# Performance work log

Measured on AMD Instinct MI355X. Metric: run time of the kernel, lower is better.

Reference implementation:

```python
import jax, jax.numpy as jnp
import numpy as np

D, H, NL, P, HP = 768, 12, 12, 16, 14          # hidden, heads, layers, patch, patches-per-side
NPATCH = HP * HP                                # 196
DH = D // H
EPS = 1e-6                                      # torchvision ViT LayerNorm eps


def _ln(x, s, b):
    m = jnp.mean(x, -1, keepdims=True)
    v = jnp.mean((x - m) ** 2, -1, keepdims=True)
    return (x - m) * jax.lax.rsqrt(v + EPS) * s + b


def _attn(x, wqkv, bqkv, wo, bo):
    B, L, _ = x.shape
    qkv = x @ wqkv + bqkv
    q, k, v = [t.reshape(B, L, H, DH) for t in jnp.split(qkv, 3, axis=-1)]
    s = jnp.einsum('bqhd,bkhd->bhqk', q, k) / np.float32(np.sqrt(DH))
    w = jax.nn.softmax(s, axis=-1)              # [B,H,L,L] per-head attn weights
    o = jnp.einsum('bhqk,bkhd->bqhd', w, v).reshape(B, L, D)
    return o @ wo + bo, w


def _block(x, i, ln1_s, ln1_b, qkv_w, qkv_b, proj_w, proj_b, ln2_s, ln2_b, mlp_w1, mlp_b1, mlp_w2, mlp_b2):
    a, _ = _attn(_ln(x, ln1_s[i], ln1_b[i]), qkv_w[i], qkv_b[i], proj_w[i], proj_b[i])
    x = x + a
    h = _ln(x, ln2_s[i], ln2_b[i])
    h = jax.nn.gelu(h @ mlp_w1[i] + mlp_b1[i], approximate=False) @ mlp_w2[i] + mlp_b2[i]
    return x + h


def setup_inputs():
    key = jax.random.key(0)
    ks = jax.random.split(key, 10)
    B, sd = 32, 0.02
    f = lambda kk, sh: jax.random.normal(kk, sh, jnp.float32) * sd
    return dict(
        x=jax.random.normal(ks[0], (B, 3, 224, 224), jnp.float32),
        conv_w=f(ks[1], (D, 3, P, P)),
        conv_b=jnp.zeros((D,), jnp.float32),
        cls_tok=f(ks[2], (1, 1, D)),
        pos_emb=f(ks[3], (1, NPATCH + 1, D)),
        ln1_s=jnp.ones((NL, D), jnp.float32), ln1_b=jnp.zeros((NL, D), jnp.float32),
        qkv_w=f(ks[4], (NL, D, 3 * D)), qkv_b=jnp.zeros((NL, 3 * D), jnp.float32),
        proj_w=f(ks[5], (NL, D, D)), proj_b=jnp.zeros((NL, D), jnp.float32),
        ln2_s=jnp.ones((NL, D), jnp.float32), ln2_b=jnp.zeros((NL, D), jnp.float32),
        mlp_w1=f(ks[6], (NL, D, 4 * D)), mlp_b1=jnp.zeros((NL, 4 * D), jnp.float32),
        mlp_w2=f(ks[7], (NL, 4 * D, D)), mlp_b2=jnp.zeros((NL, D), jnp.float32),
        fln_s=jnp.ones((D,), jnp.float32), fln_b=jnp.zeros((D,), jnp.float32),
        imp_w=f(ks[8], (D, 1)), imp_b=jnp.zeros((1,), jnp.float32),
        k=100,
    )


def reference(x, conv_w, conv_b, cls_tok, pos_emb, ln1_s, ln1_b, qkv_w, qkv_b,
              proj_w, proj_b, ln2_s, ln2_b, mlp_w1, mlp_b1, mlp_w2, mlp_b2,
              fln_s, fln_b, imp_w, imp_b, k):
    B = x.shape[0]
    # conv_proj (stride==kernel==16) as patchify + GEMM
    p = x.reshape(B, 3, HP, P, HP, P).transpose(0, 2, 4, 1, 3, 5).reshape(B, NPATCH, 3 * P * P)
    t = p @ conv_w.reshape(D, -1).T + conv_b
    t = jnp.concatenate([jnp.broadcast_to(cls_tok, (B, 1, D)), t], axis=1) + pos_emb
    blk = lambda xx, i: _block(xx, i, ln1_s, ln1_b, qkv_w, qkv_b, proj_w, proj_b,
                               ln2_s, ln2_b, mlp_w1, mlp_b1, mlp_w2, mlp_b2)
    for i in range(NL - 1):
        t = blk(t, i)
    # eager re-run of penultimate layer's self-attention on x (no pre-LN, per source)
    _, w = _attn(t, qkv_w[NL - 2], qkv_b[NL - 2], proj_w[NL - 2], proj_b[NL - 2])
    A_hat = w[:, :, 0, 1:].sum(axis=1)                       # [B, NPATCH] cls-row attn summed over heads
    patches = t[:, 1:, :]
    Z = jax.nn.sigmoid(patches @ imp_w + imp_b)[..., 0]
    O = A_hat + A_hat * Z
    _, idx = jax.lax.top_k(O, k)                             # indices (sorted desc; source uses sorted=False)
    gidx = jnp.broadcast_to(idx[:, :, None], (B, k, D))
    top_patches = jnp.take_along_axis(patches, gidx, axis=1)
    pos_full = jnp.broadcast_to(pos_emb, (B, NPATCH + 1, D))
    top_pos = jnp.take_along_axis(pos_full[:, 1:, :], gidx, axis=1)
    inp = jnp.concatenate([t[:, :1, :], top_patches], axis=1) + \
          jnp.concatenate([pos_full[:, :1, :], top_pos], axis=1)
    out = blk(inp, NL - 1)
    out = _ln(out, fln_s, fln_b)
    return out, top_patches
```

## Files before the change

### kernel.cpp

```cpp
#include <hip/hip_runtime.h>
#include <hip/hip_fp16.h>
#include <cmath>


#define NHEAD 12

typedef __attribute__((ext_vector_type(8))) _Float16 half8;
typedef __attribute__((ext_vector_type(4))) float f32x4;

__device__ __forceinline__ void split2h(float x, short& h, short& l) {
    __half hh = __float2half(x);
    float r = x - __half2float(hh);
    h = __half_as_short(hh);
    l = __half_as_short(__float2half(r));
}

__device__ __forceinline__ void ldg2lds(const void* g, void* l) {
    __builtin_amdgcn_global_load_lds((const __attribute__((address_space(1))) void*)g,
                                     (__attribute__((address_space(3))) void*)l, 16, 0, 0);
}

template<int OP>
__global__ __launch_bounds__(256, 2) void mgemm_k(
    const short* __restrict__ Ah, const short* __restrict__ Al,
    const short* __restrict__ Bh, const short* __restrict__ Bl,
    const float* __restrict__ bias, const float* __restrict__ R,
    float* __restrict__ C, short* __restrict__ Ch, short* __restrict__ Cl,
    int M, int N, int K, int ldc)
{
    __shared__ short sA[2][2][128 * 32];
    __shared__ short sB[2][2][128 * 32];
    const int tid = threadIdx.x;
    const int wid = tid >> 6, lane = tid & 63;
    const int wm = wid >> 1, wn = wid & 1;
    const int quad = lane >> 4, l15 = lane & 15;
    const int row0 = blockIdx.y * 128, col0 = blockIdx.x * 128;

    f32x4 acc[4][4];
#pragma unroll
    for (int i = 0; i < 4; ++i)
#pragma unroll
        for (int j = 0; j < 4; ++j) { acc[i][j][0] = 0.f; acc[i][j][1] = 0.f; acc[i][j][2] = 0.f; acc[i][j][3] = 0.f; }

    const int srow = lane >> 2;
    const int schunk = (lane & 3) * 8;
    const int KT = K >> 5;

    auto stage = [&](int buf, int kt) {
        int kk = kt << 5;
#pragma unroll
        for (int rnd = 0; rnd < 2; ++rnd) {
            int m = rnd * 64 + wid * 16 + srow;
            int gr = row0 + m; if (gr > M - 1) gr = M - 1;
            int gn = col0 + m;
            size_t ao = (size_t)gr * K + kk + schunk;
            size_t bo = (size_t)gn * K + kk + schunk;
            int lofs = (rnd * 64 + wid * 16) * 32;
            ldg2lds(Ah + ao, &sA[buf][0][lofs]);
            ldg2lds(Al + ao, &sA[buf][1][lofs]);
            ldg2lds(Bh + bo, &sB[buf][0][lofs]);
            ldg2lds(Bl + bo, &sB[buf][1][lofs]);
        }
    };

    stage(0, 0);
    for (int kt = 0; kt < KT; ++kt) {
        int cur = kt & 1;
        __syncthreads();
        if (kt + 1 < KT) stage(cur ^ 1, kt + 1);

        half8 a[4][2];
#pragma unroll
        for (int i = 0; i < 4; ++i) {
            int m = wm * 64 + i * 16 + l15;
#pragma unroll
            for (int p = 0; p < 2; ++p)
                a[i][p] = *(const half8*)&sA[cur][p][m * 32 + quad * 8];
        }
#pragma unroll
        for (int j = 0; j < 4; ++j) {
            int n = wn * 64 + j * 16 + l15;
            half8 bh = *(const half8*)&sB[cur][0][n * 32 + quad * 8];
            half8 bl = *(const half8*)&sB[cur][1][n * 32 + quad * 8];
#pragma unroll
            for (int i = 0; i < 4; ++i) {
                acc[i][j] = __builtin_amdgcn_mfma_f32_16x16x32_f16(a[i][1], bh, acc[i][j], 0, 0, 0);
                acc[i][j] = __builtin_amdgcn_mfma_f32_16x16x32_f16(a[i][0], bl, acc[i][j], 0, 0, 0);
                acc[i][j] = __builtin_amdgcn_mfma_f32_16x16x32_f16(a[i][0], bh, acc[i][j], 0, 0, 0);
            }
        }
    }

#pragma unroll
    for (int i = 0; i < 4; ++i) {
#pragma unroll
        for (int r = 0; r < 4; ++r) {
            int gr = row0 + wm * 64 + i * 16 + quad * 4 + r;
            if (gr >= M) continue;
#pragma unroll
            for (int j = 0; j < 4; ++j) {
                int gc = col0 + wn * 64 + j * 16 + l15;
                float v = acc[i][j][r] + bias[gc];
                if (OP == 1) v += R[(size_t)gr * ldc + gc];
                if (OP == 2) {
                    v = 0.5f * v * (1.f + erff(v * 0.70710678118654752f));
                    short h, l; split2h(v, h, l);
                    size_t o = (size_t)gr * ldc + gc;
                    Ch[o] = h; Cl[o] = l;
                } else {
                    C[(size_t)gr * ldc + gc] = v;
                }
            }
        }
    }
}

__global__ __launch_bounds__(256) void ts_k(
    const float* __restrict__ W, int ld,
    short* __restrict__ Bh, short* __restrict__ Bl, int K, int N)
{
    __shared__ float tile[32][33];
    int n0 = blockIdx.x * 32, k0 = blockIdx.y * 32;
    int c = threadIdx.x & 31, r0 = threadIdx.x >> 5;
    for (int rr = r0; rr < 32; rr += 8)
        tile[rr][c] = W[(size_t)(k0 + rr) * ld + n0 + c];
    __syncthreads();
    for (int rr = r0; rr < 32; rr += 8) {
        float v = tile[c][rr];
        short h, l; split2h(v, h, l);
        size_t o = (size_t)(n0 + rr) * K + k0 + c;
        Bh[o] = h; Bl[o] = l;
    }
}

__global__ __launch_bounds__(256) void esplit_k(
    const float* __restrict__ X, short* __restrict__ H,
    short* __restrict__ Lo, int n)
{
    int i = blockIdx.x * 256 + threadIdx.x;
    if (i < n) { short h, l; split2h(X[i], h, l); H[i] = h; Lo[i] = l; }
}

template<int MODE>
__global__ __launch_bounds__(256) void ln_k(
    const float* __restrict__ x, const float* __restrict__ s,
    const float* __restrict__ bb, float* __restrict__ y,
    short* __restrict__ yh, short* __restrict__ yl)
{
    int r = blockIdx.x;
    int tid = threadIdx.x;
    const float* xr = x + (size_t)r * 768;
    float v0 = xr[tid], v1 = xr[tid + 256], v2 = xr[tid + 512];
    __shared__ float red[256];
    red[tid] = v0 + v1 + v2;
    __syncthreads();
    for (int off = 128; off > 0; off >>= 1) {
        if (tid < off) red[tid] += red[tid + off];
        __syncthreads();
    }
    float m = red[0] / 768.f;
    __syncthreads();
    float d0 = v0 - m, d1 = v1 - m, d2 = v2 - m;
    red[tid] = d0 * d0 + d1 * d1 + d2 * d2;
    __syncthreads();
    for (int off = 128; off > 0; off >>= 1) {
        if (tid < off) red[tid] += red[tid + off];
        __syncthreads();
    }
    float inv = 1.f / sqrtf(red[0] / 768.f + 1e-6f);
    float o0 = d0 * inv * s[tid] + bb[tid];
    float o1 = d1 * inv * s[tid + 256] + bb[tid + 256];
    float o2 = d2 * inv * s[tid + 512] + bb[tid + 512];
    if (MODE == 0) {
        float* yr = y + (size_t)r * 768;
        yr[tid] = o0; yr[tid + 256] = o1; yr[tid + 512] = o2;
    } else {
        size_t base = (size_t)r * 768;
        short h, l;
        split2h(o0, h, l); yh[base + tid] = h;       yl[base + tid] = l;
        split2h(o1, h, l); yh[base + tid + 256] = h; yl[base + tid + 256] = l;
        split2h(o2, h, l); yh[base + tid + 512] = h; yl[base + tid + 512] = l;
    }
}

#define FMA8(qj, ka, kb, ac) \
    ac[0] = fmaf(qj, ka.x, ac[0]); ac[1] = fmaf(qj, ka.y, ac[1]); \
    ac[2] = fmaf(qj, ka.z, ac[2]); ac[3] = fmaf(qj, ka.w, ac[3]); \
    ac[4] = fmaf(qj, kb.x, ac[4]); ac[5] = fmaf(qj, kb.y, ac[5]); \
    ac[6] = fmaf(qj, kb.z, ac[6]); ac[7] = fmaf(qj, kb.w, ac[7]);

__global__ __launch_bounds__(256) void attn2_k(
    const float* __restrict__ qkv,
    short* __restrict__ oh, short* __restrict__ ol, int L)
{
    __shared__ __align__(16) float sKt[64 * 256];
    __shared__ __align__(16) float sV[208 * 64];
    __shared__ __align__(16) float qs[32 * 64];
    __shared__ __align__(16) float ps[224 * 36];
    __shared__ float red[8 * 32];
    __shared__ float sinv[32];

    const int tid = threadIdx.x;
    const int h = blockIdx.x, b = blockIdx.y;
    const float* base = qkv + (size_t)b * L * 2304;
    const float* qbase = base + h * 64;
    const float* kbase = base + 768 + h * 64;
    const float* vbase = base + 1536 + h * 64;

    for (int idx = tid; idx < L * 16; idx += 256) {
        int r = idx >> 4, c = (idx & 15) << 2;
        float4 kv = *(const float4*)(kbase + (size_t)r * 2304 + c);
        sKt[(c + 0) * 256 + r] = kv.x;
        sKt[(c + 1) * 256 + r] = kv.y;
        sKt[(c + 2) * 256 + r] = kv.z;
        sKt[(c + 3) * 256 + r] = kv.w;
    }
    {
        int vIters = (L * 16 + 255) >> 8;
        for (int p2 = 0; p2 < vIters; ++p2) {
            int idx = p2 * 256 + tid;
            int r = idx >> 4; if (r > L - 1) r = L - 1;
            ldg2lds(vbase + (size_t)r * 2304 + ((idx & 15) << 2), &sV[idx * 4]);
        }
    }

    const int ko = tid & 31, qq8 = tid >> 5;
    const int qsm = tid & 31, seg = tid >> 5;
    const int pq = tid & 7, dd = tid >> 3;
    const int ntiles = (L + 31) >> 5;
    const int Lr4 = (L + 3) & ~3;

    for (int t = 0; t < ntiles; ++t) {
        int q0 = t << 5;
        __syncthreads();
        {
            int idx = tid;
            int r = q0 + (idx >> 4); if (r > L - 1) r = L - 1;
            ldg2lds(qbase + (size_t)r * 2304 + ((idx & 15) << 2), &qs[idx * 4]);
            idx = 256 + tid;
            r = q0 + (idx >> 4); if (r > L - 1) r = L - 1;
            ldg2lds(qbase + (size_t)r * 2304 + ((idx & 15) << 2), &qs[idx * 4]);
        }
        __syncthreads();

        float acc[4][8];
#pragma unroll
        for (int j = 0; j < 4; ++j)
#pragma unroll
            for (int c = 0; c < 8; ++c) acc[j][c] = 0.f;

        const float* kp = &sKt[ko * 8];
#pragma unroll 4
        for (int d4 = 0; d4 < 16; ++d4) {
            float4 k0[4], k1[4];
#pragma unroll
            for (int dd2 = 0; dd2 < 4; ++dd2) {
                int d = d4 * 4 + dd2;
                k0[dd2] = *(const float4*)&kp[d * 256];
                k1[dd2] = *(const float4*)&kp[d * 256 + 4];
            }
#pragma unroll
            for (int j = 0; j < 4; ++j) {
                float4 qv = *(const float4*)&qs[(qq8 * 4 + j) * 64 + d4 * 4];
                FMA8(qv.x, k0[0], k1[0], acc[j]);
                FMA8(qv.y, k0[1], k1[1], acc[j]);
                FMA8(qv.z, k0[2], k1[2], acc[j]);
                FMA8(qv.w, k0[3], k1[3], acc[j]);
            }
        }
        {
            int chnk = ((qq8 ^ ko) & 7) << 2;
#pragma unroll
            for (int c = 0; c < 8; ++c) {
                int k2 = ko * 8 + c;
                if (k2 < 224) {
                    float4 w;
                    if (k2 < L) {
                        w.x = acc[0][c] * 0.125f; w.y = acc[1][c] * 0.125f;
                        w.z = acc[2][c] * 0.125f; w.w = acc[3][c] * 0.125f;
                    } else { w.x = -1e30f; w.y = -1e30f; w.z = -1e30f; w.w = -1e30f; }
                    *(float4*)&ps[k2 * 36 + chnk] = w;
                }
            }
        }
        __syncthreads();

        float mloc = -1e30f;
#pragma unroll 4
        for (int j2 = 0; j2 < 28; ++j2) {
            int k2 = seg * 28 + j2;
            mloc = fmaxf(mloc, ps[k2 * 36 + ((((qsm >> 2) ^ (k2 >> 3)) & 7) << 2) + (qsm & 3)]);
        }
        red[seg * 32 + qsm] = mloc;
        __syncthreads();
        float mm = red[qsm];
#pragma unroll
        for (int s2 = 1; s2 < 8; ++s2) mm = fmaxf(mm, red[s2 * 32 + qsm]);
        __syncthreads();
        float sum = 0.f;
#pragma unroll 4
        for (int j2 = 0; j2 < 28; ++j2) {
            int k2 = seg * 28 + j2;
            int o2 = k2 * 36 + ((((qsm >> 2) ^ (k2 >> 3)) & 7) << 2) + (qsm & 3);
            float e = expf(ps[o2] - mm);
            ps[o2] = e;
            sum += e;
        }
        red[seg * 32 + qsm] = sum;
        __syncthreads();
        float tot = red[qsm];
#pragma unroll
        for (int s2 = 1; s2 < 8; ++s2) tot += red[s2 * 32 + qsm];
        if (tid < 32) sinv[tid] = 1.f / tot;
        __syncthreads();

        float pacc[4][2];
#pragma unroll
        for (int j = 0; j < 4; ++j) { pacc[j][0] = 0.f; pacc[j][1] = 0.f; }
        for (int k2 = 0; k2 < Lr4; k2 += 4) {
#pragma unroll
            for (int i2 = 0; i2 < 4; ++i2) {
                int kk = k2 + i2;
                const float4 pv = *(const float4*)&ps[kk * 36 + (((pq ^ (kk >> 3)) & 7) << 2)];
                const float2 vv = *(const float2*)&sV[kk * 64 + dd * 2];
                pacc[0][0] = fmaf(pv.x, vv.x, pacc[0][0]);
                pacc[0][1] = fmaf(pv.x, vv.y, pacc[0][1]);
                pacc[1][0] = fmaf(pv.y, vv.x, pacc[1][0]);
                pacc[1][1] = fmaf(pv.y, vv.y, pacc[1][1]);
                pacc[2][0] = fmaf(pv.z, vv.x, pacc[2][0]);
                pacc[2][1] = fmaf(pv.z, vv.y, pacc[2][1]);
                pacc[3][0] = fmaf(pv.w, vv.x, pacc[3][0]);
                pacc[3][1] = fmaf(pv.w, vv.y, pacc[3][1]);
            }
        }
#pragma unroll
        for (int j = 0; j < 4; ++j) {
            int grow = q0 + pq * 4 + j;
            if (grow >= L) continue;
            float inv = sinv[pq * 4 + j];
            size_t o = ((size_t)(b * L + grow)) * 768 + h * 64 + dd * 2;
            short hh, ll;
            split2h(pacc[j][0] * inv, hh, ll);
            oh[o] = hh; ol[o] = ll;
            split2h(pacc[j][1] * inv, hh, ll);
            oh[o + 1] = hh; ol[o + 1] = ll;
        }
    }
}

__global__ __launch_bounds__(256) void gather_k(
    const float* __restrict__ x,
    short* __restrict__ ph, short* __restrict__ pl)
{
    int n = blockIdx.x, b = blockIdx.y, tid = threadIdx.x;
    int hp = n / 14, wp = n % 14;
    size_t base = ((size_t)(b * 196 + n)) * 768;
    for (int e = tid; e < 768; e += 256) {
        int c = e >> 8, rem = e & 255, rr = rem >> 4, cc = rem & 15;
        float v = x[((size_t)(b * 3 + c) * 224 + (hp * 16 + rr)) * 224 + wp * 16 + cc];
        short h, l; split2h(v, h, l);
        ph[base + e] = h; pl[base + e] = l;
    }
}

__global__ __launch_bounds__(256) void embed_k(
    const float* __restrict__ tpatch, const float* __restrict__ cls,
    const float* __restrict__ pos, float* __restrict__ t)
{
    int m = blockIdx.x, b = blockIdx.y, tid = threadIdx.x;
    float* dst = t + ((size_t)(b * 197 + m)) * 768;
    if (m == 0) {
        for (int e = tid; e < 768; e += 256) dst[e] = cls[e] + pos[e];
    } else {
        const float* s2 = tpatch + ((size_t)(b * 196 + m - 1)) * 768;
        for (int e = tid; e < 768; e += 256) dst[e] = s2[e] + pos[(size_t)m * 768 + e];
    }
}

__global__ __launch_bounds__(256) void q0_k(
    const float* __restrict__ T, const float* __restrict__ W,
    const float* __restrict__ bq, float* __restrict__ q0)
{
    int b = blockIdx.x, tid = threadIdx.x;
    __shared__ float ys[768];
    const float* yr = T + (size_t)b * 197 * 768;
    ys[tid] = yr[tid]; ys[tid + 256] = yr[tid + 256]; ys[tid + 512] = yr[tid + 512];
    __syncthreads();
    for (int d = tid; d < 768; d += 256) {
        float acc = bq[d];
        for (int k2 = 0; k2 < 768; ++k2) acc += ys[k2] * W[(size_t)k2 * 2304 + d];
        q0[(size_t)b * 768 + d] = acc;
    }
}

__global__ __launch_bounds__(256) void ahat_k(
    const float* __restrict__ kmat, const float* __restrict__ q0,
    float* __restrict__ Ahat)
{
    int b = blockIdx.x, tid = threadIdx.x;
    __shared__ float qs[64];
    __shared__ float sc[256];
    __shared__ float red[256];
    __shared__ float ah[196];
    for (int j = tid; j < 196; j += 256) ah[j] = 0.f;
    for (int h = 0; h < NHEAD; ++h) {
        __syncthreads();
        if (tid < 64) qs[tid] = q0[(size_t)b * 768 + h * 64 + tid];
        __syncthreads();
        if (tid < 197) {
            const float* kr = kmat + ((size_t)(b * 197 + tid)) * 768 + h * 64;
            float acc = 0.f;
            for (int d = 0; d < 64; ++d) acc += qs[d] * kr[d];
            sc[tid] = acc * 0.125f;
        }
        __syncthreads();
        red[tid] = (tid < 197) ? sc[tid] : -1e30f;
        __syncthreads();
        for (int off = 128; off > 0; off >>= 1) {
            if (tid < off) red[tid] = fmaxf(red[tid], red[tid + off]);
            __syncthreads();
        }
        float m = red[0];
        __syncthreads();
        float e = 0.f;
        if (tid < 197) { e = expf(sc[tid] - m); sc[tid] = e; }
        red[tid] = e;
        __syncthreads();
        for (int off = 128; off > 0; off >>= 1) {
            if (tid < off) red[tid] += red[tid + off];
            __syncthreads();
        }
        float inv = 1.f / red[0];
        if (tid >= 1 && tid < 197) ah[tid - 1] += sc[tid] * inv;
    }
    __syncthreads();
    for (int j = tid; j < 196; j += 256) Ahat[(size_t)b * 196 + j] = ah[j];
}

__global__ __launch_bounds__(256) void zo_k(
    const float* __restrict__ t, const float* __restrict__ impw,
    const float* __restrict__ impb, const float* __restrict__ Ahat,
    float* __restrict__ O)
{
    int b = blockIdx.x, tid = threadIdx.x;
    __shared__ float w[768];
    w[tid] = impw[tid]; w[tid + 256] = impw[tid + 256]; w[tid + 512] = impw[tid + 512];
    __syncthreads();
    for (int j = tid; j < 196; j += 256) {
        const float* tr = t + ((size_t)(b * 197) + 1 + j) * 768;
        float acc = impb[0];
        for (int d = 0; d < 768; ++d) acc += tr[d] * w[d];
        float z = 1.f / (1.f + expf(-acc));
        float a = Ahat[(size_t)b * 196 + j];
        O[(size_t)b * 196 + j] = a + a * z;
    }
}

__global__ __launch_bounds__(256) void topk_k(const float* __restrict__ O, int* __restrict__ idx)
{
    int b = blockIdx.x, tid = threadIdx.x;
    __shared__ float s[196];
    if (tid < 196) s[tid] = O[(size_t)b * 196 + tid];
    __syncthreads();
    if (tid < 196) {
        float v = s[tid];
        int rank = 0;
        for (int i = 0; i < 196; ++i) {
            float u = s[i];
            rank += (u > v) || (u == v && i < tid);
        }
        if (rank < 100) idx[b * 100 + rank] = tid;
    }
}

__global__ __launch_bounds__(256) void build_k(
    const float* __restrict__ t, const float* __restrict__ pos,
    const int* __restrict__ idx, float* __restrict__ inp, float* __restrict__ tp)
{
    int m = blockIdx.x, b = blockIdx.y, tid = threadIdx.x;
    float* dst = inp + ((size_t)(b * 101 + m)) * 768;
    if (m == 0) {
        const float* tr = t + (size_t)b * 197 * 768;
        for (int e = tid; e < 768; e += 256) dst[e] = tr[e] + pos[e];
    } else {
        int j = idx[b * 100 + m - 1];
        const float* tr = t + ((size_t)(b * 197) + 1 + j) * 768;
        const float* pr = pos + (size_t)(1 + j) * 768;
        float* tpr = tp + ((size_t)(b * 100) + (m - 1)) * 768;
        for (int e = tid; e < 768; e += 256) {
            float val = tr[e];
            tpr[e] = val;
            dst[e] = val + pr[e];
        }
    }
}

extern "C" void kernel_launch(void* const* d_in, const int* in_sizes, int n_in,
                              void* d_out, int out_size, void* d_ws, size_t ws_size,
                              hipStream_t stream)
{
    const float* x      = (const float*)d_in[0];
    const float* conv_w = (const float*)d_in[1];
    const float* conv_b = (const float*)d_in[2];
    const float* cls    = (const float*)d_in[3];
    const float* pos    = (const float*)d_in[4];
    const float* ln1_s  = (const float*)d_in[5];
    const float* ln1_b  = (const float*)d_in[6];
    const float* qkv_w  = (const float*)d_in[7];
    const float* qkv_b  = (const float*)d_in[8];
    const float* proj_w = (const float*)d_in[9];
    const float* proj_b = (const float*)d_in[10];
    const float* ln2_s  = (const float*)d_in[11];
    const float* ln2_b  = (const float*)d_in[12];
    const float* mlp_w1 = (const float*)d_in[13];
    const float* mlp_b1 = (const float*)d_in[14];
    const float* mlp_w2 = (const float*)d_in[15];
    const float* mlp_b2 = (const float*)d_in[16];
    const float* fln_s  = (const float*)d_in[17];
    const float* fln_b  = (const float*)d_in[18];
    const float* imp_w  = (const float*)d_in[19];
    const float* imp_b  = (const float*)d_in[20];

    const size_t SZ_T = (size_t)32 * 197 * 768;
    const size_t SZ_H = (size_t)32 * 197 * 3072;
    const size_t SZ_W = (size_t)768 * 3072;

    char* p = (char*)d_ws;
    auto alloc = [&](size_t bytes) { char* r = p; p += (bytes + 255) & ~(size_t)255; return r; };
    float* T   = (float*)alloc(SZ_T * 4);
    float* INP = (float*)alloc((size_t)32 * 101 * 768 * 4);
    float* Q0  = (float*)alloc(24576 * 4);
    float* AH  = (float*)alloc(6272 * 4);
    float* OV  = (float*)alloc(6272 * 4);
    int*   IDX = (int*)alloc(3200 * 4);
    short* Yh  = (short*)alloc(SZ_T * 2);
    short* Yl  = (short*)alloc(SZ_T * 2);
    short* Wh  = (short*)alloc(SZ_W * 2);
    short* Wl  = (short*)alloc(SZ_W * 2);
    char*  S   = alloc((size_t)116195328);
    float* QKV = (float*)S;
    short* OBh = (short*)(S + (size_t)58097664);
    short* OBl = OBh + SZ_T;
    short* Hh = (short*)S;
    short* Hl = Hh + SZ_H;

    float* out0 = (float*)d_out;
    float* out1 = out0 + (size_t)32 * 101 * 768;

    auto cvt = [&](const float* W, int K, int N, int ld) {
        ts_k<<<dim3(N / 32, K / 32), 256, 0, stream>>>(W, ld, Wh, Wl, K, N);
    };

    esplit_k<<<(768 * 768) / 256, 256, 0, stream>>>(conv_w, Wh, Wl, 768 * 768);
    gather_k<<<dim3(196, 32), 256, 0, stream>>>(x, Yh, Yl);
    mgemm_k<0><<<dim3(6, 49), 256, 0, stream>>>(Yh, Yl, Wh, Wl, conv_b, nullptr,
                                                QKV, nullptr, nullptr, 6272, 768, 768, 768);
    embed_k<<<dim3(197, 32), 256, 0, stream>>>(QKV, cls, pos, T);

    auto run_block = [&](float* X, int L, int i) {
        int M = 32 * L;
        int mt = (M + 127) / 128;
        ln_k<1><<<M, 256, 0, stream>>>(X, ln1_s + i * 768, ln1_b + i * 768, nullptr, Yh, Yl);
        cvt(qkv_w + (size_t)i * 768 * 2304, 768, 2304, 2304);
        mgemm_k<0><<<dim3(18, mt), 256, 0, stream>>>(Yh, Yl, Wh, Wl, qkv_b + (size_t)i * 2304,
                                                     nullptr, QKV, nullptr, nullptr, M, 2304, 768, 2304);
        attn2_k<<<dim3(NHEAD, 32), 256, 0, stream>>>(QKV, OBh, OBl, L);
        cvt(proj_w + (size_t)i * 768 * 768, 768, 768, 768);
        mgemm_k<1><<<dim3(6, mt), 256, 0, stream>>>(OBh, OBl, Wh, Wl, proj_b + (size_t)i * 768,
                                                    X, X, nullptr, nullptr, M, 768, 768, 768);
        ln_k<1><<<M, 256, 0, stream>>>(X, ln2_s + i * 768, ln2_b + i * 768, nullptr, Yh, Yl);
        cvt(mlp_w1 + (size_t)i * 768 * 3072, 768, 3072, 3072);
        mgemm_k<2><<<dim3(24, mt), 256, 0, stream>>>(Yh, Yl, Wh, Wl, mlp_b1 + (size_t)i * 3072,
                                                     nullptr, nullptr, Hh, Hl, M, 3072, 768, 3072);
        cvt(mlp_w2 + (size_t)i * 3072 * 768, 3072, 768, 768);
        mgemm_k<1><<<dim3(6, mt), 256, 0, stream>>>(Hh, Hl, Wh, Wl, mlp_b2 + (size_t)i * 768,
                                                    X, X, nullptr, nullptr, M, 768, 3072, 768);
    };

    for (int i = 0; i < 11; ++i) run_block(T, 197, i);

    esplit_k<<<(int)(SZ_T / 256), 256, 0, stream>>>(T, Yh, Yl, (int)SZ_T);
    cvt(qkv_w + (size_t)10 * 768 * 2304 + 768, 768, 768, 2304);
    mgemm_k<0><<<dim3(6, 50), 256, 0, stream>>>(Yh, Yl, Wh, Wl, qkv_b + (size_t)10 * 2304 + 768,
                                                nullptr, QKV, nullptr, nullptr, 6304, 768, 768, 768);
    q0_k<<<32, 256, 0, stream>>>(T, qkv_w + (size_t)10 * 768 * 2304, qkv_b + (size_t)10 * 2304, Q0);
    ahat_k<<<32, 256, 0, stream>>>(QKV, Q0, AH);
    zo_k<<<32, 256, 0, stream>>>(T, imp_w, imp_b, AH, OV);
    topk_k<<<32, 256, 0, stream>>>(OV, IDX);
    build_k<<<dim3(101, 32), 256, 0, stream>>>(T, pos, IDX, INP, out1);

    run_block(INP, 101, 11);

    ln_k<0><<<32 * 101, 256, 0, stream>>>(INP, fln_s, fln_b, out0, nullptr, nullptr);

    (void)in_sizes; (void)n_in; (void)out_size; (void)ws_size;
}
```

Before: 8.329 ms.

## Split attention query tiles across two blocks and store K row-major

Replaces the attention kernel with a templated version that splits the query-tile loop across two blocks per (head, batch) using a third grid dimension, doubling the block count. K is stored row-major with a padded stride instead of transposed, and each thread handles keys strided by 32 with a compile-time count. The score-matrix swizzle is dropped in favour of a direct layout. In exchange, each block still loads the full K and V, duplicating that load work, and the new LDS layouts may introduce bank conflicts.

Result: faster. 7.741 ms (-7.1%).

```diff
diff --git a/kernel.cpp b/kernel.cpp
--- a/kernel.cpp
+++ b/kernel.cpp
@@ -183,17 +183,12 @@
     }
 }
 
-#define FMA8(qj, ka, kb, ac) \
-    ac[0] = fmaf(qj, ka.x, ac[0]); ac[1] = fmaf(qj, ka.y, ac[1]); \
-    ac[2] = fmaf(qj, ka.z, ac[2]); ac[3] = fmaf(qj, ka.w, ac[3]); \
-    ac[4] = fmaf(qj, kb.x, ac[4]); ac[5] = fmaf(qj, kb.y, ac[5]); \
-    ac[6] = fmaf(qj, kb.z, ac[6]); ac[7] = fmaf(qj, kb.w, ac[7]);
-
-__global__ __launch_bounds__(256) void attn2_k(
+template<int CMAX>
+__global__ __launch_bounds__(256) void attn3_k(
     const float* __restrict__ qkv,
     short* __restrict__ oh, short* __restrict__ ol, int L)
 {
-    __shared__ __align__(16) float sKt[64 * 256];
+    __shared__ __align__(16) float sK[224 * 68];
     __shared__ __align__(16) float sV[208 * 64];
     __shared__ __align__(16) float qs[32 * 64];
     __shared__ __align__(16) float ps[224 * 36];
@@ -201,7 +196,7 @@
     __shared__ float sinv[32];
 
     const int tid = threadIdx.x;
-    const int h = blockIdx.x, b = blockIdx.y;
+    const int h = blockIdx.x, b = blockIdx.y, z = blockIdx.z;
     const float* base = qkv + (size_t)b * L * 2304;
     const float* qbase = base + h * 64;
     const float* kbase = base + 768 + h * 64;
@@ -209,11 +204,7 @@
 
     for (int idx = tid; idx < L * 16; idx += 256) {
         int r = idx >> 4, c = (idx & 15) << 2;
-        float4 kv = *(const float4*)(kbase + (size_t)r * 2304 + c);
-        sKt[(c + 0) * 256 + r] = kv.x;
-        sKt[(c + 1) * 256 + r] = kv.y;
-        sKt[(c + 2) * 256 + r] = kv.z;
-        sKt[(c + 3) * 256 + r] = kv.w;
+        *(float4*)&sK[r * 68 + c] = *(const float4*)(kbase + (size_t)r * 2304 + c);
     }
     {
         int vIters = (L * 16 + 255) >> 8;
@@ -229,8 +220,9 @@
     const int pq = tid & 7, dd = tid >> 3;
     const int ntiles = (L + 31) >> 5;
     const int Lr4 = (L + 3) & ~3;
-
-    for (int t = 0; t < ntiles; ++t) {
+    const int rps = CMAX * 4;
+
+    for (int t = z; t < ntiles; t += 2) {
         int q0 = t << 5;
         __syncthreads();
         {
@@ -243,54 +235,46 @@
         }
         __syncthreads();
 
-        float acc[4][8];
-#pragma unroll
-        for (int j = 0; j < 4; ++j)
-#pragma unroll
-            for (int c = 0; c < 8; ++c) acc[j][c] = 0.f;
-
-        const float* kp = &sKt[ko * 8];
+        float acc[CMAX][4];
+#pragma unroll
+        for (int c = 0; c < CMAX; ++c)
+#pragma unroll
+            for (int j = 0; j < 4; ++j) acc[c][j] = 0.f;
+
 #pragma unroll 4
         for (int d4 = 0; d4 < 16; ++d4) {
-            float4 k0[4], k1[4];
-#pragma unroll
-            for (int dd2 = 0; dd2 < 4; ++dd2) {
-                int d = d4 * 4 + dd2;
-                k0[dd2] = *(const float4*)&kp[d * 256];
-                k1[dd2] = *(const float4*)&kp[d * 256 + 4];
-            }
+            float4 kv[CMAX];
+#pragma unroll
+            for (int c = 0; c < CMAX; ++c)
+                kv[c] = *(const float4*)&sK[(ko + 32 * c) * 68 + d4 * 4];
 #pragma unroll
             for (int j = 0; j < 4; ++j) {
                 float4 qv = *(const float4*)&qs[(qq8 * 4 + j) * 64 + d4 * 4];
-                FMA8(qv.x, k0[0], k1[0], acc[j]);
-                FMA8(qv.y, k0[1], k1[1], acc[j]);
-                FMA8(qv.z, k0[2], k1[2], acc[j]);
-                FMA8(qv.w, k0[3], k1[3], acc[j]);
-            }
-        }
-        {
-            int chnk = ((qq8 ^ ko) & 7) << 2;
-#pragma unroll
-            for (int c = 0; c < 8; ++c) {
-                int k2 = ko * 8 + c;
-                if (k2 < 224) {
-                    float4 w;
-                    if (k2 < L) {
-                        w.x = acc[0][c] * 0.125f; w.y = acc[1][c] * 0.125f;
-                        w.z = acc[2][c] * 0.125f; w.w = acc[3][c] * 0.125f;
-                    } else { w.x = -1e30f; w.y = -1e30f; w.z = -1e30f; w.w = -1e30f; }
-                    *(float4*)&ps[k2 * 36 + chnk] = w;
+#pragma unroll
+                for (int c = 0; c < CMAX; ++c) {
+                    acc[c][j] = fmaf(qv.x, kv[c].x, acc[c][j]);
+                    acc[c][j] = fmaf(qv.y, kv[c].y, acc[c][j]);
+                    acc[c][j] = fmaf(qv.z, kv[c].z, acc[c][j]);
+                    acc[c][j] = fmaf(qv.w, kv[c].w, acc[c][j]);
                 }
             }
         }
+#pragma unroll
+        for (int c = 0; c < CMAX; ++c) {
+            int k2 = ko + 32 * c;
+            float4 w;
+            if (k2 < L) {
+                w.x = acc[c][0] * 0.125f; w.y = acc[c][1] * 0.125f;
+                w.z = acc[c][2] * 0.125f; w.w = acc[c][3] * 0.125f;
+            } else { w.x = -1e30f; w.y = -1e30f; w.z = -1e30f; w.w = -1e30f; }
+            *(float4*)&ps[k2 * 36 + qq8 * 4] = w;
+        }
         __syncthreads();
 
         float mloc = -1e30f;
 #pragma unroll 4
-        for (int j2 = 0; j2 < 28; ++j2) {
-            int k2 = seg * 28 + j2;
-            mloc = fmaxf(mloc, ps[k2 * 36 + ((((qsm >> 2) ^ (k2 >> 3)) & 7) << 2) + (qsm & 3)]);
-        }
+        for (int j2 = 0; j2 < rps; ++j2)
+            mloc = fmaxf(mloc, ps[(seg * rps + j2) * 36 + qsm]);
         red[seg * 32 + qsm] = mloc;
         __syncthreads();
         float mm = red[qsm];
@@ -299,9 +283,8 @@
         __syncthreads();
         float sum = 0.f;
 #pragma unroll 4
-        for (int j2 = 0; j2 < 28; ++j2) {
-            int k2 = seg * 28 + j2;
-            int o2 = k2 * 36 + ((((qsm >> 2) ^ (k2 >> 3)) & 7) << 2) + (qsm & 3);
+        for (int j2 = 0; j2 < rps; ++j2) {
+            int o2 = (seg * rps + j2) * 36 + qsm;
             float e = expf(ps[o2] - mm);
             ps[o2] = e;
             sum += e;
@@ -321,7 +304,7 @@
 #pragma unroll
             for (int i2 = 0; i2 < 4; ++i2) {
                 int kk = k2 + i2;
-                const float4 pv = *(const float4*)&ps[kk * 36 + (((pq ^ (kk >> 3)) & 7) << 2)];
+                const float4 pv = *(const float4*)&ps[kk * 36 + pq * 4];
                 const float2 vv = *(const float2*)&sV[kk * 64 + dd * 2];
                 pacc[0][0] = fmaf(pv.x, vv.x, pacc[0][0]);
                 pacc[0][1] = fmaf(pv.x, vv.y, pacc[0][1]);
@@ -564,7 +547,10 @@
         cvt(qkv_w + (size_t)i * 768 * 2304, 768, 2304, 2304);
         mgemm_k<0><<<dim3(18, mt), 256, 0, stream>>>(Yh, Yl, Wh, Wl, qkv_b + (size_t)i * 2304,
                                                      nullptr, QKV, nullptr, nullptr, M, 2304, 768, 2304);
-        attn2_k<<<dim3(NHEAD, 32), 256, 0, stream>>>(QKV, OBh, OBl, L);
+        if (L == 197)
+            attn3_k<7><<<dim3(NHEAD, 32, 2), 256, 0, stream>>>(QKV, OBh, OBl, L);
+        else
+            attn3_k<4><<<dim3(NHEAD, 32, 2), 256, 0, stream>>>(QKV, OBh, OBl, L);
         cvt(proj_w + (size_t)i * 768 * 768, 768, 768, 768);
         mgemm_k<1><<<dim3(6, mt), 256, 0, stream>>>(OBh, OBl, Wh, Wl, proj_b + (size_t)i * 768,
                                                     X, X, nullptr, nullptr, M, 768, 768, 768);
```
